# Kernel tuning notes

Hardware: AMD Instinct MI355X
Metric: run time of the kernel (lower is better)

## Reference

```python
import jax, jax.numpy as jnp
import numpy as np

N_FEATURES = 60
WINDOW = 64
N_FFT_BINS = WINDOW // 2 + 1  # 33
HIDDEN = 256
N_OUT = 3
TOTAL_IN = N_FEATURES + N_FEATURES * N_FFT_BINS  # 2040


def setup_inputs() -> dict:
    key = jax.random.key(0)
    ks = jax.random.split(key, 9)
    B, T = 4, 4096
    x = jax.random.normal(ks[0], (B, T, N_FEATURES), dtype=jnp.float32)

    def lin(k, fan_in, fan_out):
        bound = 1.0 / np.sqrt(fan_in)
        kw, kb = jax.random.split(k)
        W = jax.random.uniform(kw, (fan_in, fan_out), minval=-bound, maxval=bound, dtype=jnp.float32)
        b = jax.random.uniform(kb, (fan_out,), minval=-bound, maxval=bound, dtype=jnp.float32)
        return W, b

    W1, b1 = lin(ks[1], TOTAL_IN, HIDDEN)
    W2, b2 = lin(ks[2], HIDDEN, HIDDEN)
    W3, b3 = lin(ks[3], HIDDEN, HIDDEN // 2)
    W4, b4 = lin(ks[4], HIDDEN // 2, N_OUT)
    return {"x": x, "W1": W1, "b1": b1, "W2": W2, "b2": b2,
            "W3": W3, "b3": b3, "W4": W4, "b4": b4}


def _fft_features(x):
    # x: [B, T, F]
    B, T, F = x.shape
    half_w = WINDOW // 2
    # reflect pad along time: (half_w, half_w - 1)
    xp = jnp.pad(x, ((0, 0), (half_w, half_w - 1), (0, 0)), mode='reflect')  # [B, T+W-1, F]
    # sliding windows: [B, T, W, F] -> [B, T, F, W] (matches torch unfold layout)
    idx = jnp.arange(T)[:, None] + jnp.arange(WINDOW)[None, :]  # [T, W]
    windows = xp[:, idx, :].transpose(0, 1, 3, 2)  # [B, T, F, W]
    fft_mag = jnp.log1p(jnp.abs(jnp.fft.rfft(windows, axis=-1)))  # [B, T, F, W//2+1]
    return fft_mag.reshape(B, T, F * N_FFT_BINS)


def reference(x, W1, b1, W2, b2, W3, b3, W4, b4):
    fft_flat = _fft_features(x)
    h = jnp.concatenate([x, fft_flat], axis=-1)  # [B, T, 2040]
    h = jax.nn.relu(h @ W1 + b1)   # dropout is identity in eval mode
    h = jax.nn.relu(h @ W2 + b2)
    h = jax.nn.relu(h @ W3 + b3)
    return h @ W4 + b4             # [B, T, 3]
```

## Files before the change

### kernel.cpp

```cpp
#include <hip/hip_runtime.h>
#include <math.h>

#define T_LEN 4096
#define NF 60
#define NBINS 33
#define KPAD 2048
#define HID 256
#define NTOK 16384
#define LINE 4208

typedef _Float16 half_t;
typedef half_t half8 __attribute__((ext_vector_type(8)));
typedef half_t half4 __attribute__((ext_vector_type(4)));
typedef float f32x4 __attribute__((ext_vector_type(4)));

constexpr double K_PI = 3.14159265358979323846;
constexpr double tcos(double x) {
    while (x >  K_PI) x -= 2.0 * K_PI;
    while (x < -K_PI) x += 2.0 * K_PI;
    double x2 = x * x, s = 0.0, term = 1.0;
    for (int m = 0; m < 14; ++m) { s += term; term *= -x2 / ((2.0*m + 1.0) * (2.0*m + 2.0)); }
    return s;
}
struct CosTab { float v[64]; };
constexpr CosTab make_tab() {
    CosTab t{};
    for (int j = 0; j < 64; ++j) t.v[j] = (float)tcos(2.0 * K_PI * (double)j / 64.0);
    return t;
}
__device__ constexpr CosTab CTd = make_tab();

__device__ __forceinline__ float log2_1p(float x) {
    return __log2f(1.0f + x);
}

__global__ __launch_bounds__(256) void prep_kernel(
        const float* __restrict__ W1, const float* __restrict__ W2,
        const float* __restrict__ W3,
        half_t* __restrict__ dftH,
        half_t* __restrict__ W1T, half_t* __restrict__ W2T,
        half_t* __restrict__ W3T) {
    int i = blockIdx.x * 256 + threadIdx.x;
    if (i < 4096) {
        int row = i >> 6, n = i & 63;
        float c = (row < 33) ? CTd.v[(row * n) & 63]
                             : CTd.v[((row - 32) * n + 48) & 63];
        dftH[i] = (half_t)c;
        return;
    }
    i -= 4096;
    if (i < 256 * KPAD) {
        int gk = i & (KPAD - 1);
        float v = 0.f;
        if (gk < 2040) {
            int j = i >> 11;
            int r;
            bool isfft = true;
            if (gk < 1920) {
                int f = gk >> 5, bin = gk & 31;
                r = NF + f * NBINS + bin;
            } else if (gk < 1980) {
                r = gk - 1920; isfft = false;
            } else {
                r = NF + (gk - 1980) * NBINS + 32;
            }
            v = W1[(size_t)r * HID + j];
            if (isfft) v *= 0.69314718055994531f;
        }
        W1T[i] = (half_t)v;
        return;
    }
    i -= 256 * KPAD;
    if (i < 256 * 256) {
        int k = i & 255, j = i >> 8;
        W2T[i] = (half_t)W2[(size_t)k * HID + j];
        return;
    }
    i -= 256 * 256;
    if (i < 128 * 256) {
        int k = i & 255, j = i >> 8;
        W3T[i] = (half_t)W3[(size_t)k * 128 + j];
    }
}

__global__ __launch_bounds__(256) void xline_kernel(
        const float* __restrict__ x, half_t* __restrict__ lineG) {
    const int bf = blockIdx.x;
    const int b = bf / NF, f = bf - b * NF;
    const float* xb = x + (size_t)b * T_LEN * NF + f;
    half_t* L = lineG + (size_t)bf * LINE;
    for (int j = threadIdx.x; j < LINE; j += 256) {
        int s = j - 32;
        int r = (s < 0) ? -s : ((s > T_LEN - 1) ? 2 * (T_LEN - 1) - s : s);
        L[j] = (half_t)xb[(size_t)r * NF];
    }
}

__global__ __launch_bounds__(256) void raw_kernel(
        const float* __restrict__ x, half_t* __restrict__ H0) {
    const int t = blockIdx.x * 256 + threadIdx.x;
    const int b = t >> 12, tl = t & (T_LEN - 1);
    const int i = (b << 12) + ((tl & 7) << 9) + (tl >> 3);
    const float* xp = x + (size_t)t * NF;
    half_t* hp = H0 + (size_t)i * KPAD;
#pragma unroll
    for (int f4 = 0; f4 < 15; ++f4) {
        float4 v = *(const float4*)(xp + f4 * 4);
        half4 h;
        h[0] = (half_t)v.x; h[1] = (half_t)v.y;
        h[2] = (half_t)v.z; h[3] = (half_t)v.w;
        *(half4*)&hp[1920 + f4 * 4] = h;
    }
    half8 z = {};
    *(half8*)&hp[2040] = z;
}

__global__ __launch_bounds__(256) void fft_hankel(
        const half_t* __restrict__ lineG, const half_t* __restrict__ dftH,
        half_t* __restrict__ H0) {
    __shared__ half_t L[2176];

    const int bid = blockIdx.x;
    const int bf = bid >> 4, c = (bid >> 1) & 7, hf = bid & 1;
    const int b = bf / NF, f = bf - b * NF;
    const int tid = threadIdx.x;
    const int lane = tid & 63, wv = tid >> 6;
    const int lr = lane & 15, lg = lane >> 4;

    half8 a[4][2];
#pragma unroll
    for (int rf = 0; rf < 4; ++rf)
#pragma unroll
        for (int ks = 0; ks < 2; ++ks)
            a[rf][ks] = *(const half8*)&dftH[(16 * rf + lr) * 64 + ks * 32 + lg * 8];

    {
        const half_t* src = lineG + (size_t)bf * LINE + hf * 2048 + c;
        for (int j = tid; j < 2144; j += 256) L[j] = src[j];
    }
    __syncthreads();

    const int i0 = (b << 12) + (c << 9) + (hf << 8);

#pragma unroll
    for (int cs = 0; cs < 4; ++cs) {
        const int s0 = wv * 64 + cs * 16;
        half8 w0 = *(const half8*)&L[8 * (s0 + lr) + lg * 8];
        half8 w1 = *(const half8*)&L[8 * (s0 + lr) + 32 + lg * 8];
        f32x4 dacc[4] = {};
#pragma unroll
        for (int rf = 0; rf < 4; ++rf)
            dacc[rf] = __builtin_amdgcn_mfma_f32_16x16x32_f16(a[rf][0], w0, dacc[rf], 0, 0, 0);
#pragma unroll
        for (int rf = 0; rf < 4; ++rf)
            dacc[rf] = __builtin_amdgcn_mfma_f32_16x16x32_f16(a[rf][1], w1, dacc[rf], 0, 0, 0);

        half_t* base = H0 + (size_t)(i0 + s0 + lr) * KPAD;
#pragma unroll
        for (int rf = 0; rf < 2; ++rf) {
            half4 h4;
#pragma unroll
            for (int r = 0; r < 4; ++r) {
                float re = dacc[rf][r];
                float im = dacc[rf + 2][r];
                float v = (rf == 0 && r == 0)
                    ? ((lg == 0) ? log2_1p(fabsf(re))
                                 : log2_1p(sqrtf(re * re + im * im)))
                    : log2_1p(sqrtf(re * re + im * im));
                h4[r] = (half_t)v;
            }
            *(half4*)&base[f * 32 + 16 * rf + 4 * lg] = h4;
        }
        if (lg == 0)
            base[1980 + f] = (half_t)log2_1p(fabsf(dacc[2][0]));
    }
}

template<int BN, bool OUT_F32>
__global__ __launch_bounds__(256, 2) void gemm_bdir(
        const half_t* __restrict__ A, int lda,
        const half_t* __restrict__ BT, int ldb,
        const float* __restrict__ bias,
        half_t* __restrict__ Ch, float* __restrict__ Cf,
        int N, int K) {
    constexpr int NFR = BN / 64;
    __shared__ half_t As[2][64][72];

    const int tid  = threadIdx.x;
    const int row0 = blockIdx.x * 64;
    const int col0 = blockIdx.y * BN;
    const int wv = tid >> 6, lane = tid & 63;
    const int lr = lane & 15, lg = lane >> 4;

    const int arow = tid >> 2, ak = (tid & 3) * 16;
    const half_t* ap = A + (size_t)(row0 + arow) * lda + ak;

    f32x4 acc[4][NFR] = {};
    const int NIT = K / 64;

    {
        half8 v0 = *(const half8*)(ap);
        half8 v1 = *(const half8*)(ap + 8);
        *(half8*)&As[0][arow][ak]     = v0;
        *(half8*)&As[0][arow][ak + 8] = v1;
    }

    for (int it = 0; it < NIT; ++it) {
        const int cur = it & 1;
        half8 av0, av1;
        if (it + 1 < NIT) {
            av0 = *(const half8*)(ap + (it + 1) * 64);
            av1 = *(const half8*)(ap + (it + 1) * 64 + 8);
        }
        __syncthreads();
        const int k0 = it * 64;
#pragma unroll
        for (int ks = 0; ks < 2; ++ks) {
            half8 af[4], bf[NFR];
#pragma unroll
            for (int mf = 0; mf < 4; ++mf)
                af[mf] = *(const half8*)&As[cur][mf * 16 + lr][ks * 32 + lg * 8];
#pragma unroll
            for (int nf = 0; nf < NFR; ++nf) {
                int col = col0 + wv * (16 * NFR) + nf * 16 + lr;
                bf[nf] = *(const half8*)&BT[(size_t)col * ldb + k0 + ks * 32 + lg * 8];
            }
#pragma unroll
            for (int mf = 0; mf < 4; ++mf)
#pragma unroll
                for (int nf = 0; nf < NFR; ++nf)
                    acc[mf][nf] = __builtin_amdgcn_mfma_f32_16x16x32_f16(af[mf], bf[nf], acc[mf][nf], 0, 0, 0);
        }
        if (it + 1 < NIT) {
            *(half8*)&As[cur ^ 1][arow][ak]     = av0;
            *(half8*)&As[cur ^ 1][arow][ak + 8] = av1;
        }
    }

#pragma unroll
    for (int nf = 0; nf < NFR; ++nf) {
        int col = col0 + wv * (16 * NFR) + nf * 16 + lr;
        float bs = bias[col];
#pragma unroll
        for (int mf = 0; mf < 4; ++mf)
#pragma unroll
            for (int r = 0; r < 4; ++r) {
                int row = row0 + mf * 16 + lg * 4 + r;
                float v = fmaxf(acc[mf][nf][r] + bs, 0.f);
                if (OUT_F32) Cf[(size_t)row * N + col] = v;
                else         Ch[(size_t)row * N + col] = (half_t)v;
            }
    }
}

__global__ __launch_bounds__(256) void head_kernel(
        const float* __restrict__ H, const float* __restrict__ W4,
        const float* __restrict__ b4, float* __restrict__ out) {
    __shared__ float Ws[128 * 3];
    __shared__ float bs[3];
    for (int i = threadIdx.x; i < 384; i += 256) Ws[i] = W4[i];
    if (threadIdx.x < 3) bs[threadIdx.x] = b4[threadIdx.x];
    __syncthreads();
    const int i = blockIdx.x * 256 + threadIdx.x;
    const float* h = H + (size_t)i * 128;
    float a0 = bs[0], a1 = bs[1], a2 = bs[2];
#pragma unroll
    for (int k = 0; k < 128; ++k) {
        float hv = h[k];
        a0 = fmaf(hv, Ws[k * 3 + 0], a0);
        a1 = fmaf(hv, Ws[k * 3 + 1], a1);
        a2 = fmaf(hv, Ws[k * 3 + 2], a2);
    }
    const int b = i >> 12, c = (i >> 9) & 7, s = i & 511;
    const int t = (b << 12) + (s << 3) + c;
    float* o = out + (size_t)t * 3;
    o[0] = a0; o[1] = a1; o[2] = a2;
}

extern "C" void kernel_launch(void* const* d_in, const int* in_sizes, int n_in,
                              void* d_out, int out_size, void* d_ws, size_t ws_size,
                              hipStream_t stream) {
    (void)in_sizes; (void)n_in; (void)out_size; (void)ws_size;
    const float* x  = (const float*)d_in[0];
    const float* W1 = (const float*)d_in[1];
    const float* b1 = (const float*)d_in[2];
    const float* W2 = (const float*)d_in[3];
    const float* b2 = (const float*)d_in[4];
    const float* W3 = (const float*)d_in[5];
    const float* b3 = (const float*)d_in[6];
    const float* W4 = (const float*)d_in[7];
    const float* b4 = (const float*)d_in[8];
    float* out = (float*)d_out;

    char* w = (char*)d_ws;
    half_t* H0    = (half_t*)(w);
    half_t* H1    = (half_t*)(w + (size_t)64 * 1024 * 1024);
    half_t* H2    = (half_t*)(w + (size_t)72 * 1024 * 1024);
    float*  H3    = (float*) (w + (size_t)80 * 1024 * 1024);
    half_t* W1T   = (half_t*)(w + (size_t)88 * 1024 * 1024);
    half_t* W2T   = (half_t*)(w + (size_t)89 * 1024 * 1024);
    half_t* W3T   = W2T + 256 * 256;
    half_t* dftH  = W3T + 128 * 256;
    half_t* lineG = (half_t*)(w + (size_t)90 * 1024 * 1024);

    prep_kernel<<<2448, 256, 0, stream>>>(W1, W2, W3, dftH, W1T, W2T, W3T);
    xline_kernel<<<240, 256, 0, stream>>>(x, lineG);
    raw_kernel<<<NTOK / 256, 256, 0, stream>>>(x, H0);
    fft_hankel<<<240 * 16, 256, 0, stream>>>(lineG, dftH, H0);

    gemm_bdir<128, false><<<dim3(NTOK / 64, 2), 256, 0, stream>>>(
        H0, KPAD, W1T, KPAD, b1, H1, nullptr, HID, KPAD);
    gemm_bdir<128, false><<<dim3(NTOK / 64, 2), 256, 0, stream>>>(
        H1, HID, W2T, HID, b2, H2, nullptr, HID, HID);
    gemm_bdir<64, true><<<dim3(NTOK / 64, 2), 256, 0, stream>>>(
        H2, HID, W3T, HID, b3, nullptr, H3, HID / 2, HID);

    head_kernel<<<NTOK / 256, 256, 0, stream>>>(H3, W4, b4, out);
}
```

Measured before the change: 125.1 us.

## Software-pipeline GEMM with register-prefetched B fragments and XOR-swizzled LDS

Restructures the MLP GEMM main loop. The loop is unrolled by two K-steps, and the B (weight) fragments for the next step are prefetched into registers while the current step's MFMAs run. A tiles are prefetched two stages ahead from global memory. The padded LDS tile is replaced by an unpadded 64x64 layout with an XOR swizzle to avoid bank conflicts. This aims to hide global load latency for B and shrink LDS use, at the cost of more registers, which could reduce occupancy under the launch bounds of 2 blocks.

Measured after the change: 117.3 us. 6.2% less time.

```diff
diff --git a/kernel.cpp b/kernel.cpp
--- a/kernel.cpp
+++ b/kernel.cpp
@@ -177,14 +177,14 @@
 }
 
 template<int BN, bool OUT_F32>
-__global__ __launch_bounds__(256, 2) void gemm_bdir(
+__global__ __launch_bounds__(256, 2) void gemm_pipe(
         const half_t* __restrict__ A, int lda,
         const half_t* __restrict__ BT, int ldb,
         const float* __restrict__ bias,
         half_t* __restrict__ Ch, float* __restrict__ Cf,
         int N, int K) {
     constexpr int NFR = BN / 64;
-    __shared__ half_t As[2][64][72];
+    __shared__ half_t As[2][64 * 64];
 
     const int tid  = threadIdx.x;
     const int row0 = blockIdx.x * 64;
@@ -192,49 +192,83 @@
     const int wv = tid >> 6, lane = tid & 63;
     const int lr = lane & 15, lg = lane >> 4;
 
-    const int arow = tid >> 2, ak = (tid & 3) * 16;
-    const half_t* ap = A + (size_t)(row0 + arow) * lda + ak;
+    const int srow = tid >> 2, sg = (tid & 3) * 2;
+    const int wo0 = srow * 64 + ((sg ^ (srow & 7)) * 8);
+    const int wo1 = srow * 64 + (((sg + 1) ^ (srow & 7)) * 8);
+    const half_t* ap = A + (size_t)(row0 + srow) * lda + sg * 8;
+
+    const half_t* bp[NFR];
+#pragma unroll
+    for (int nf = 0; nf < NFR; ++nf)
+        bp[nf] = BT + (size_t)(col0 + wv * (16 * NFR) + nf * 16 + lr) * ldb + lg * 8;
 
     f32x4 acc[4][NFR] = {};
     const int NIT = K / 64;
+
+    half8 bcur[2][NFR], bnxt[2][NFR];
+    half8 pa0, pa1, pb0, pb1;
 
     {
         half8 v0 = *(const half8*)(ap);
         half8 v1 = *(const half8*)(ap + 8);
-        *(half8*)&As[0][arow][ak]     = v0;
-        *(half8*)&As[0][arow][ak + 8] = v1;
-    }
-
-    for (int it = 0; it < NIT; ++it) {
-        const int cur = it & 1;
-        half8 av0, av1;
+        *(half8*)&As[0][wo0] = v0;
+        *(half8*)&As[0][wo1] = v1;
+    }
+    if (NIT > 1) { pa0 = *(const half8*)(ap + 64);  pa1 = *(const half8*)(ap + 72); }
+    if (NIT > 2) { pb0 = *(const half8*)(ap + 128); pb1 = *(const half8*)(ap + 136); }
+#pragma unroll
+    for (int ks = 0; ks < 2; ++ks)
+#pragma unroll
+        for (int nf = 0; nf < NFR; ++nf)
+            bcur[ks][nf] = *(const half8*)(bp[nf] + ks * 32);
+
+    for (int it = 0; it < NIT; it += 2) {
+        __syncthreads();
         if (it + 1 < NIT) {
-            av0 = *(const half8*)(ap + (it + 1) * 64);
-            av1 = *(const half8*)(ap + (it + 1) * 64 + 8);
-        }
+#pragma unroll
+            for (int ks = 0; ks < 2; ++ks)
+#pragma unroll
+                for (int nf = 0; nf < NFR; ++nf)
+                    bnxt[ks][nf] = *(const half8*)(bp[nf] + (it + 1) * 64 + ks * 32);
+        }
+#pragma unroll
+        for (int ks = 0; ks < 2; ++ks) {
+            half8 af[4];
+#pragma unroll
+            for (int mf = 0; mf < 4; ++mf)
+                af[mf] = *(const half8*)&As[0][(mf * 16 + lr) * 64 + (((ks * 4 + lg) ^ (lr & 7)) * 8)];
+#pragma unroll
+            for (int mf = 0; mf < 4; ++mf)
+#pragma unroll
+                for (int nf = 0; nf < NFR; ++nf)
+                    acc[mf][nf] = __builtin_amdgcn_mfma_f32_16x16x32_f16(af[mf], bcur[ks][nf], acc[mf][nf], 0, 0, 0);
+        }
+        if (it + 1 < NIT) { *(half8*)&As[1][wo0] = pa0; *(half8*)&As[1][wo1] = pa1; }
+        if (it + 3 < NIT) { pa0 = *(const half8*)(ap + (it + 3) * 64); pa1 = *(const half8*)(ap + (it + 3) * 64 + 8); }
+        if (it + 1 >= NIT) break;
+
         __syncthreads();
-        const int k0 = it * 64;
+        if (it + 2 < NIT) {
+#pragma unroll
+            for (int ks = 0; ks < 2; ++ks)
+#pragma unroll
+                for (int nf = 0; nf < NFR; ++nf)
+                    bcur[ks][nf] = *(const half8*)(bp[nf] + (it + 2) * 64 + ks * 32);
+        }
 #pragma unroll
         for (int ks = 0; ks < 2; ++ks) {
-            half8 af[4], bf[NFR];
+            half8 af[4];
 #pragma unroll
             for (int mf = 0; mf < 4; ++mf)
-                af[mf] = *(const half8*)&As[cur][mf * 16 + lr][ks * 32 + lg * 8];
-#pragma unroll
-            for (int nf = 0; nf < NFR; ++nf) {
-                int col = col0 + wv * (16 * NFR) + nf * 16 + lr;
-                bf[nf] = *(const half8*)&BT[(size_t)col * ldb + k0 + ks * 32 + lg * 8];
-            }
+                af[mf] = *(const half8*)&As[1][(mf * 16 + lr) * 64 + (((ks * 4 + lg) ^ (lr & 7)) * 8)];
 #pragma unroll
             for (int mf = 0; mf < 4; ++mf)
 #pragma unroll
                 for (int nf = 0; nf < NFR; ++nf)
-                    acc[mf][nf] = __builtin_amdgcn_mfma_f32_16x16x32_f16(af[mf], bf[nf], acc[mf][nf], 0, 0, 0);
-        }
-        if (it + 1 < NIT) {
-            *(half8*)&As[cur ^ 1][arow][ak]     = av0;
-            *(half8*)&As[cur ^ 1][arow][ak + 8] = av1;
-        }
+                    acc[mf][nf] = __builtin_amdgcn_mfma_f32_16x16x32_f16(af[mf], bnxt[ks][nf], acc[mf][nf], 0, 0, 0);
+        }
+        if (it + 2 < NIT) { *(half8*)&As[0][wo0] = pb0; *(half8*)&As[0][wo1] = pb1; }
+        if (it + 4 < NIT) { pb0 = *(const half8*)(ap + (it + 4) * 64); pb1 = *(const half8*)(ap + (it + 4) * 64 + 8); }
     }
 
 #pragma unroll
@@ -308,11 +342,11 @@
     raw_kernel<<<NTOK / 256, 256, 0, stream>>>(x, H0);
     fft_hankel<<<240 * 16, 256, 0, stream>>>(lineG, dftH, H0);
 
-    gemm_bdir<128, false><<<dim3(NTOK / 64, 2), 256, 0, stream>>>(
+    gemm_pipe<128, false><<<dim3(NTOK / 64, 2), 256, 0, stream>>>(
         H0, KPAD, W1T, KPAD, b1, H1, nullptr, HID, KPAD);
-    gemm_bdir<128, false><<<dim3(NTOK / 64, 2), 256, 0, stream>>>(
+    gemm_pipe<128, false><<<dim3(NTOK / 64, 2), 256, 0, stream>>>(
         H1, HID, W2T, HID, b2, H2, nullptr, HID, HID);
-    gemm_bdir<64, true><<<dim3(NTOK / 64, 2), 256, 0, stream>>>(
+    gemm_pipe<64, true><<<dim3(NTOK / 64, 2), 256, 0, stream>>>(
         H2, HID, W3T, HID, b3, nullptr, H3, HID / 2, HID);
 
     head_kernel<<<NTOK / 256, 256, 0, stream>>>(H3, W4, b4, out);
```
